# Kernel tuning notes

Measured on AMD Instinct MI355X. Metric: run time of the kernel, lower is better.

Reference implementation:

```python
import jax, jax.numpy as jnp
import numpy as np

N_NODES = 100000


def gcn_conv(h, edge_index, W, b):
    """PyG GCNConv: add self-loops, symmetric normalization, linear transform,
    sum aggregation over incoming edges, plus bias."""
    n = h.shape[0]
    loop = jnp.arange(n)
    row = jnp.concatenate([edge_index[0], loop])  # source nodes
    col = jnp.concatenate([edge_index[1], loop])  # destination nodes
    # degree of destination nodes (edge weight = 1)
    deg = jax.ops.segment_sum(jnp.ones_like(col, dtype=h.dtype), col, num_segments=n)
    dinv = jnp.where(deg > 0, jax.lax.rsqrt(deg), 0.0)
    norm = dinv[row] * dinv[col]  # [E+n]
    hW = h @ W                    # [n, out] small GEMM
    msg = hW[row] * norm[:, None] # gather + scale, [E+n, out]
    out = jax.ops.segment_sum(msg, col, num_segments=n)  # scatter-add
    return out + b


def setup_inputs() -> dict:
    key = jax.random.key(0)
    k1, k2, k3, k4 = jax.random.split(key, 4)
    N, E, D_IN, D_H, D_OUT = N_NODES, 1600000, 64, 64, 32
    x = jax.random.normal(k1, (N, D_IN), dtype=jnp.float32)
    edge_index = jax.random.randint(k2, (2, E), 0, N, dtype=jnp.int64)
    W1 = jax.random.normal(k3, (D_IN, D_H), dtype=jnp.float32) / np.sqrt(D_IN)
    b1 = jnp.zeros((D_H,), dtype=jnp.float32)
    W2 = jax.random.normal(k4, (D_H, D_OUT), dtype=jnp.float32) / np.sqrt(D_H)
    b2 = jnp.zeros((D_OUT,), dtype=jnp.float32)
    return {"x": x, "edge_index": edge_index, "W1": W1, "b1": b1, "W2": W2, "b2": b2}


def reference(x, edge_index, W1, b1, W2, b2):
    # StackedGCNEncoder.encode, eval mode (dropout is identity at inference)
    h = gcn_conv(x, edge_index, W1, b1)
    h = jax.nn.relu(h)
    h = gcn_conv(h, edge_index, W2, b2)
    return h
```

## Files before the change

### kernel.cpp

```cpp
#include <hip/hip_runtime.h>

#define NN 100000
#define NNr 100016
#define NE 1600000
#define STRIDE 48

static __device__ __forceinline__ unsigned short f2bf(float f) {
    unsigned int u = __float_as_uint(f);
    return (unsigned short)((u + 0x7FFFu + ((u >> 16) & 1u)) >> 16);
}
static __device__ __forceinline__ float bflo(unsigned int u) {
    return __uint_as_float(u << 16);
}
static __device__ __forceinline__ float bfhi(unsigned int u) {
    return __uint_as_float(u & 0xFFFF0000u);
}

__global__ void zero_k(int* __restrict__ a, int n) {
    int i = blockIdx.x * blockDim.x + threadIdx.x;
    if (i < n) a[i] = 0;
}

__global__ void dinv_k(const int* __restrict__ cursor, float* __restrict__ dinv, int n) {
    int i = blockIdx.x * blockDim.x + threadIdx.x;
    if (i < n) dinv[i] = rsqrtf((float)cursor[i] + 1.0f);
}

__global__ __launch_bounds__(256) void fused1_k(const float* __restrict__ x,
        const float* __restrict__ W1, unsigned short* __restrict__ A,
        const int* __restrict__ ei, int* __restrict__ cursor,
        int* __restrict__ csr) {
    __shared__ __align__(16) float smem[32 * 68 + 64 * 64];

    if (blockIdx.x & 1) {
        int i = (int)(blockIdx.x >> 1) * 256 + threadIdx.x;
        int2 s = *reinterpret_cast<const int2*>(ei + 2 * i);
        int2 d = *reinterpret_cast<const int2*>(ei + NE + 2 * i);
        int p0 = atomicAdd(&cursor[d.x], 1);
        if (p0 < STRIDE) csr[d.x * STRIDE + p0] = s.x;
        int p1 = atomicAdd(&cursor[d.y], 1);
        if (p1 < STRIDE) csr[d.y * STRIDE + p1] = s.y;
        return;
    }

    float* sH = smem;
    float* sW = smem + 32 * 68;
    const int row0 = (int)(blockIdx.x >> 1) * 32;

    for (int i = threadIdx.x; i < 16 * 64; i += 256)
        *reinterpret_cast<float4*>(&sW[i * 4]) = reinterpret_cast<const float4*>(W1)[i];
    for (int t = threadIdx.x; t < 32 * 16; t += 256) {
        int r = t >> 4, k4 = (t & 15) << 2;
        *reinterpret_cast<float4*>(&sH[r * 68 + k4]) =
            *reinterpret_cast<const float4*>(x + (long long)(row0 + r) * 64 + k4);
    }
    __syncthreads();

    const int tc = threadIdx.x & 15, tr = threadIdx.x >> 4;
    const int rb = tr * 2, cb = tc * 4;
    float acc[2][4] = {};
#pragma unroll
    for (int k = 0; k < 64; k += 4) {
        float a[2][4], w[4][4];
#pragma unroll
        for (int i = 0; i < 2; ++i) {
            float4 t4 = *reinterpret_cast<const float4*>(&sH[(rb + i) * 68 + k]);
            a[i][0] = t4.x; a[i][1] = t4.y; a[i][2] = t4.z; a[i][3] = t4.w;
        }
#pragma unroll
        for (int kk = 0; kk < 4; ++kk) {
            float4 t4 = *reinterpret_cast<const float4*>(&sW[(k + kk) * 64 + cb]);
            w[kk][0] = t4.x; w[kk][1] = t4.y; w[kk][2] = t4.z; w[kk][3] = t4.w;
        }
#pragma unroll
        for (int i = 0; i < 2; ++i)
#pragma unroll
            for (int kk = 0; kk < 4; ++kk)
#pragma unroll
                for (int j = 0; j < 4; ++j)
                    acc[i][j] = fmaf(a[i][kk], w[kk][j], acc[i][j]);
    }
#pragma unroll
    for (int i = 0; i < 2; ++i) {
        ushort4 o;
        o.x = f2bf(acc[i][0]); o.y = f2bf(acc[i][1]);
        o.z = f2bf(acc[i][2]); o.w = f2bf(acc[i][3]);
        *reinterpret_cast<ushort4*>(A + (long long)(row0 + rb + i) * 64 + cb) = o;
    }
}

__global__ __launch_bounds__(256) void gather_gemm2_k(const int* __restrict__ cursor,
        const int* __restrict__ csr, const unsigned int* __restrict__ A32,
        const float* __restrict__ dinv, const float* __restrict__ b1,
        const float* __restrict__ W2, unsigned short* __restrict__ C, int n) {
    __shared__ __align__(16) float sW2[64 * 32];
    __shared__ float sB[4][64];

    for (int i = threadIdx.x; i < 16 * 32; i += 256)
        *reinterpret_cast<float4*>(&sW2[i * 4]) = reinterpret_cast<const float4*>(W2)[i];
    __syncthreads();

    const int wv = threadIdx.x >> 6, lane = threadIdx.x & 63;
    const int half = lane >> 5;
    const int fl = lane & 31;
    const int v = blockIdx.x * 4 + wv;
    if (v >= n) return;

    const int beg = v * STRIDE;
    const int end = beg + min(cursor[v], STRIDE);
    const float dv = dinv[v];
    const unsigned int av = A32[(long long)v * 32 + fl];

    float m0 = 0.0f, m1 = 0.0f;
    int p = beg + half;
    while (p + 6 < end) {
        int r0 = csr[p], r1 = csr[p + 2], r2 = csr[p + 4], r3 = csr[p + 6];
        float n0 = dinv[r0], n1 = dinv[r1], n2 = dinv[r2], n3 = dinv[r3];
        unsigned int a0 = A32[(long long)r0 * 32 + fl];
        unsigned int a1 = A32[(long long)r1 * 32 + fl];
        unsigned int a2 = A32[(long long)r2 * 32 + fl];
        unsigned int a3 = A32[(long long)r3 * 32 + fl];
        m0 = fmaf(bflo(a0), n0, m0); m1 = fmaf(bfhi(a0), n0, m1);
        m0 = fmaf(bflo(a1), n1, m0); m1 = fmaf(bfhi(a1), n1, m1);
        m0 = fmaf(bflo(a2), n2, m0); m1 = fmaf(bfhi(a2), n2, m1);
        m0 = fmaf(bflo(a3), n3, m0); m1 = fmaf(bfhi(a3), n3, m1);
        p += 8;
    }
    while (p < end) {
        int r = csr[p];
        float nr = dinv[r];
        unsigned int a = A32[(long long)r * 32 + fl];
        m0 = fmaf(bflo(a), nr, m0); m1 = fmaf(bfhi(a), nr, m1);
        p += 2;
    }
    m0 += __shfl_xor(m0, 32);
    m1 += __shfl_xor(m1, 32);

    if (half == 0) {
        float2 bb = reinterpret_cast<const float2*>(b1)[fl];
        float B0 = fmaf(dv, fmaf(dv, bflo(av), m0), bb.x);
        float B1 = fmaf(dv, fmaf(dv, bfhi(av), m1), bb.y);
        float2 o; o.x = fmaxf(B0, 0.0f); o.y = fmaxf(B1, 0.0f);
        *reinterpret_cast<float2*>(&sB[wv][2 * fl]) = o;
    }
    __builtin_amdgcn_wave_barrier();

    const int j = lane & 31, kbase = (lane >> 5) << 5;
    float pj = 0.0f;
#pragma unroll
    for (int t = 0; t < 32; ++t) {
        int k = kbase + t;
        pj = fmaf(sB[wv][k], sW2[k * 32 + j], pj);
    }
    pj += __shfl_down(pj, 32);
    if (lane < 32) C[(long long)v * 32 + j] = f2bf(pj);
}

__global__ __launch_bounds__(256) void gather2_k(const int* __restrict__ cursor,
        const int* __restrict__ csr, const unsigned int* __restrict__ C32,
        const float* __restrict__ dinv, const float* __restrict__ b2,
        float* __restrict__ outp, int n) {
    const int wv = threadIdx.x >> 6, lane = threadIdx.x & 63;
    const int q = lane >> 4, fl = lane & 15;
    const int v = blockIdx.x * 4 + wv;
    if (v >= n) return;

    const int beg = v * STRIDE;
    const int end = beg + min(cursor[v], STRIDE);
    const float dv = dinv[v];
    const unsigned int cv = C32[(long long)v * 16 + fl];

    float m0 = 0.0f, m1 = 0.0f;
    int p = beg + q;
    while (p + 12 < end) {
        int r0 = csr[p], r1 = csr[p + 4], r2 = csr[p + 8], r3 = csr[p + 12];
        float n0 = dinv[r0], n1 = dinv[r1], n2 = dinv[r2], n3 = dinv[r3];
        unsigned int c0 = C32[(long long)r0 * 16 + fl];
        unsigned int c1 = C32[(long long)r1 * 16 + fl];
        unsigned int c2 = C32[(long long)r2 * 16 + fl];
        unsigned int c3 = C32[(long long)r3 * 16 + fl];
        m0 = fmaf(bflo(c0), n0, m0); m1 = fmaf(bfhi(c0), n0, m1);
        m0 = fmaf(bflo(c1), n1, m0); m1 = fmaf(bfhi(c1), n1, m1);
        m0 = fmaf(bflo(c2), n2, m0); m1 = fmaf(bfhi(c2), n2, m1);
        m0 = fmaf(bflo(c3), n3, m0); m1 = fmaf(bfhi(c3), n3, m1);
        p += 16;
    }
    while (p < end) {
        int r = csr[p];
        float nr = dinv[r];
        unsigned int c = C32[(long long)r * 16 + fl];
        m0 = fmaf(bflo(c), nr, m0); m1 = fmaf(bfhi(c), nr, m1);
        p += 4;
    }
    m0 += __shfl_xor(m0, 16); m0 += __shfl_xor(m0, 32);
    m1 += __shfl_xor(m1, 16); m1 += __shfl_xor(m1, 32);

    if (q == 0) {
        float2 bb = reinterpret_cast<const float2*>(b2)[fl];
        float2 o;
        o.x = fmaf(dv, fmaf(dv, bflo(cv), m0), bb.x);
        o.y = fmaf(dv, fmaf(dv, bfhi(cv), m1), bb.y);
        reinterpret_cast<float2*>(outp)[(long long)v * 16 + fl] = o;
    }
}

extern "C" void kernel_launch(void* const* d_in, const int* in_sizes, int n_in,
                              void* d_out, int out_size, void* d_ws, size_t ws_size,
                              hipStream_t stream) {
    const float* x  = (const float*)d_in[0];
    const int*   ei = (const int*)d_in[1];
    const float* W1 = (const float*)d_in[2];
    const float* b1 = (const float*)d_in[3];
    const float* W2 = (const float*)d_in[4];
    const float* b2 = (const float*)d_in[5];
    float* out = (float*)d_out;

    int*            cursor = (int*)d_ws;
    int*            csr    = cursor + NNr;
    float*          dinv   = (float*)(csr + NN * STRIDE);
    unsigned short* A      = (unsigned short*)(dinv + NNr);
    unsigned short* C      = A + (long long)NN * 64;

    const int BT = 256;

    zero_k<<<(NN + BT - 1) / BT, BT, 0, stream>>>(cursor, NN);
    fused1_k<<<6250, BT, 0, stream>>>(x, W1, A, ei, cursor, csr);
    dinv_k<<<(NN + BT - 1) / BT, BT, 0, stream>>>(cursor, dinv, NN);
    gather_gemm2_k<<<(NN + 3) / 4, BT, 0, stream>>>(cursor, csr,
        (const unsigned int*)A, dinv, b1, W2, C, NN);
    gather2_k<<<(NN + 3) / 4, BT, 0, stream>>>(cursor, csr,
        (const unsigned int*)C, dinv, b2, out, NN);
}
```

Baseline: 188.8 us.

## Pre-scale features by source dinv and load CSR indices once per wave

Replaces the dinv kernel with a scale pass that multiplies the bf16 hW rows by rsqrt(deg+1) in place. The second layer folds dv into the stored C rows, so neither gather has to fetch dinv[r] for each edge. Each wave also loads its node's CSR row once into lanes and broadcasts indices with shuffles, instead of issuing dependent csr loads per iteration. This drops one random gather per edge, at the cost of an extra read-modify-write over A and a second bf16 rounding of the scaled values.

Result: faster. 174.8 us (-7.4%).

```diff
diff --git a/kernel.cpp b/kernel.cpp
--- a/kernel.cpp
+++ b/kernel.cpp
@@ -15,15 +15,13 @@
 static __device__ __forceinline__ float bfhi(unsigned int u) {
     return __uint_as_float(u & 0xFFFF0000u);
 }
+static __device__ __forceinline__ unsigned int bfpack(float lo, float hi) {
+    return ((unsigned int)f2bf(lo)) | (((unsigned int)f2bf(hi)) << 16);
+}
 
 __global__ void zero_k(int* __restrict__ a, int n) {
     int i = blockIdx.x * blockDim.x + threadIdx.x;
     if (i < n) a[i] = 0;
-}
-
-__global__ void dinv_k(const int* __restrict__ cursor, float* __restrict__ dinv, int n) {
-    int i = blockIdx.x * blockDim.x + threadIdx.x;
-    if (i < n) dinv[i] = rsqrtf((float)cursor[i] + 1.0f);
 }
 
 __global__ __launch_bounds__(256) void fused1_k(const float* __restrict__ x,
@@ -89,10 +87,24 @@
     }
 }
 
+__global__ __launch_bounds__(256) void scale_k(unsigned int* __restrict__ A32,
+        const int* __restrict__ cursor, int n) {
+    int gid = blockIdx.x * blockDim.x + threadIdx.x;
+    if (gid >= n * 8) return;
+    int row = gid >> 3, c = gid & 7;
+    float di = rsqrtf((float)cursor[row] + 1.0f);
+    uint4 u = reinterpret_cast<uint4*>(A32)[(long long)row * 8 + c];
+    u.x = bfpack(bflo(u.x) * di, bfhi(u.x) * di);
+    u.y = bfpack(bflo(u.y) * di, bfhi(u.y) * di);
+    u.z = bfpack(bflo(u.z) * di, bfhi(u.z) * di);
+    u.w = bfpack(bflo(u.w) * di, bfhi(u.w) * di);
+    reinterpret_cast<uint4*>(A32)[(long long)row * 8 + c] = u;
+}
+
 __global__ __launch_bounds__(256) void gather_gemm2_k(const int* __restrict__ cursor,
         const int* __restrict__ csr, const unsigned int* __restrict__ A32,
-        const float* __restrict__ dinv, const float* __restrict__ b1,
-        const float* __restrict__ W2, unsigned short* __restrict__ C, int n) {
+        const float* __restrict__ b1, const float* __restrict__ W2,
+        unsigned short* __restrict__ C, int n) {
     __shared__ __align__(16) float sW2[64 * 32];
     __shared__ float sB[4][64];
 
@@ -106,41 +118,40 @@
     const int v = blockIdx.x * 4 + wv;
     if (v >= n) return;
 
-    const int beg = v * STRIDE;
-    const int end = beg + min(cursor[v], STRIDE);
-    const float dv = dinv[v];
+    const int cv = cursor[v];
+    const int deg = min(cv, STRIDE);
+    const float dv = rsqrtf((float)cv + 1.0f);
+
+    int rl = 0;
+    if (lane < deg) rl = csr[v * STRIDE + lane];
+
     const unsigned int av = A32[(long long)v * 32 + fl];
 
     float m0 = 0.0f, m1 = 0.0f;
-    int p = beg + half;
-    while (p + 6 < end) {
-        int r0 = csr[p], r1 = csr[p + 2], r2 = csr[p + 4], r3 = csr[p + 6];
-        float n0 = dinv[r0], n1 = dinv[r1], n2 = dinv[r2], n3 = dinv[r3];
-        unsigned int a0 = A32[(long long)r0 * 32 + fl];
-        unsigned int a1 = A32[(long long)r1 * 32 + fl];
-        unsigned int a2 = A32[(long long)r2 * 32 + fl];
-        unsigned int a3 = A32[(long long)r3 * 32 + fl];
-        m0 = fmaf(bflo(a0), n0, m0); m1 = fmaf(bfhi(a0), n0, m1);
-        m0 = fmaf(bflo(a1), n1, m0); m1 = fmaf(bfhi(a1), n1, m1);
-        m0 = fmaf(bflo(a2), n2, m0); m1 = fmaf(bfhi(a2), n2, m1);
-        m0 = fmaf(bflo(a3), n3, m0); m1 = fmaf(bfhi(a3), n3, m1);
-        p += 8;
-    }
-    while (p < end) {
-        int r = csr[p];
-        float nr = dinv[r];
-        unsigned int a = A32[(long long)r * 32 + fl];
-        m0 = fmaf(bflo(a), nr, m0); m1 = fmaf(bfhi(a), nr, m1);
-        p += 2;
+    const int T = (deg + 7) >> 3;
+    for (int it = 0; it < T; ++it) {
+        const int e0 = it * 8 + half;
+        int r0 = __shfl(rl, e0);
+        int r1 = __shfl(rl, e0 + 2);
+        int r2 = __shfl(rl, e0 + 4);
+        int r3 = __shfl(rl, e0 + 6);
+        unsigned int a0 = (e0     < deg) ? A32[(long long)r0 * 32 + fl] : 0u;
+        unsigned int a1 = (e0 + 2 < deg) ? A32[(long long)r1 * 32 + fl] : 0u;
+        unsigned int a2 = (e0 + 4 < deg) ? A32[(long long)r2 * 32 + fl] : 0u;
+        unsigned int a3 = (e0 + 6 < deg) ? A32[(long long)r3 * 32 + fl] : 0u;
+        m0 += bflo(a0); m1 += bfhi(a0);
+        m0 += bflo(a1); m1 += bfhi(a1);
+        m0 += bflo(a2); m1 += bfhi(a2);
+        m0 += bflo(a3); m1 += bfhi(a3);
     }
     m0 += __shfl_xor(m0, 32);
     m1 += __shfl_xor(m1, 32);
 
     if (half == 0) {
         float2 bb = reinterpret_cast<const float2*>(b1)[fl];
-        float B0 = fmaf(dv, fmaf(dv, bflo(av), m0), bb.x);
-        float B1 = fmaf(dv, fmaf(dv, bfhi(av), m1), bb.y);
-        float2 o; o.x = fmaxf(B0, 0.0f); o.y = fmaxf(B1, 0.0f);
+        float2 o;
+        o.x = fmaxf(fmaf(dv, m0 + bflo(av), bb.x), 0.0f);
+        o.y = fmaxf(fmaf(dv, m1 + bfhi(av), bb.y), 0.0f);
         *reinterpret_cast<float2*>(&sB[wv][2 * fl]) = o;
     }
     __builtin_amdgcn_wave_barrier();
@@ -153,44 +164,42 @@
         pj = fmaf(sB[wv][k], sW2[k * 32 + j], pj);
     }
     pj += __shfl_down(pj, 32);
-    if (lane < 32) C[(long long)v * 32 + j] = f2bf(pj);
+    if (lane < 32) C[(long long)v * 32 + j] = f2bf(pj * dv);
 }
 
 __global__ __launch_bounds__(256) void gather2_k(const int* __restrict__ cursor,
         const int* __restrict__ csr, const unsigned int* __restrict__ C32,
-        const float* __restrict__ dinv, const float* __restrict__ b2,
-        float* __restrict__ outp, int n) {
+        const float* __restrict__ b2, float* __restrict__ outp, int n) {
     const int wv = threadIdx.x >> 6, lane = threadIdx.x & 63;
     const int q = lane >> 4, fl = lane & 15;
     const int v = blockIdx.x * 4 + wv;
     if (v >= n) return;
 
-    const int beg = v * STRIDE;
-    const int end = beg + min(cursor[v], STRIDE);
-    const float dv = dinv[v];
-    const unsigned int cv = C32[(long long)v * 16 + fl];
-
+    const int cv = cursor[v];
+    const int deg = min(cv, STRIDE);
+    const float dv = rsqrtf((float)cv + 1.0f);
+
+    int rl = 0;
+    if (lane < deg) rl = csr[v * STRIDE + lane];
+
+    const unsigned int cvu = C32[(long long)v * 16 + fl];
     float m0 = 0.0f, m1 = 0.0f;
-    int p = beg + q;
-    while (p + 12 < end) {
-        int r0 = csr[p], r1 = csr[p + 4], r2 = csr[p + 8], r3 = csr[p + 12];
-        float n0 = dinv[r0], n1 = dinv[r1], n2 = dinv[r2], n3 = dinv[r3];
-        unsigned int c0 = C32[(long long)r0 * 16 + fl];
-        unsigned int c1 = C32[(long long)r1 * 16 + fl];
-        unsigned int c2 = C32[(long long)r2 * 16 + fl];
-        unsigned int c3 = C32[(long long)r3 * 16 + fl];
-        m0 = fmaf(bflo(c0), n0, m0); m1 = fmaf(bfhi(c0), n0, m1);
-        m0 = fmaf(bflo(c1), n1, m0); m1 = fmaf(bfhi(c1), n1, m1);
-        m0 = fmaf(bflo(c2), n2, m0); m1 = fmaf(bfhi(c2), n2, m1);
-        m0 = fmaf(bflo(c3), n3, m0); m1 = fmaf(bfhi(c3), n3, m1);
-        p += 16;
-    }
-    while (p < end) {
-        int r = csr[p];
-        float nr = dinv[r];
-        unsigned int c = C32[(long long)r * 16 + fl];
-        m0 = fmaf(bflo(c), nr, m0); m1 = fmaf(bfhi(c), nr, m1);
-        p += 4;
+
+    const int T = (deg + 15) >> 4;
+    for (int it = 0; it < T; ++it) {
+        const int e0 = it * 16 + q;
+        int r0 = __shfl(rl, e0);
+        int r1 = __shfl(rl, e0 + 4);
+        int r2 = __shfl(rl, e0 + 8);
+        int r3 = __shfl(rl, e0 + 12);
+        unsigned int c0 = (e0      < deg) ? C32[(long long)r0 * 16 + fl] : 0u;
+        unsigned int c1 = (e0 + 4  < deg) ? C32[(long long)r1 * 16 + fl] : 0u;
+        unsigned int c2 = (e0 + 8  < deg) ? C32[(long long)r2 * 16 + fl] : 0u;
+        unsigned int c3 = (e0 + 12 < deg) ? C32[(long long)r3 * 16 + fl] : 0u;
+        m0 += bflo(c0); m1 += bfhi(c0);
+        m0 += bflo(c1); m1 += bfhi(c1);
+        m0 += bflo(c2); m1 += bfhi(c2);
+        m0 += bflo(c3); m1 += bfhi(c3);
     }
     m0 += __shfl_xor(m0, 16); m0 += __shfl_xor(m0, 32);
     m1 += __shfl_xor(m1, 16); m1 += __shfl_xor(m1, 32);
@@ -198,8 +207,8 @@
     if (q == 0) {
         float2 bb = reinterpret_cast<const float2*>(b2)[fl];
         float2 o;
-        o.x = fmaf(dv, fmaf(dv, bflo(cv), m0), bb.x);
-        o.y = fmaf(dv, fmaf(dv, bfhi(cv), m1), bb.y);
+        o.x = fmaf(dv, m0 + bflo(cvu), bb.x);
+        o.y = fmaf(dv, m1 + bfhi(cvu), bb.y);
         reinterpret_cast<float2*>(outp)[(long long)v * 16 + fl] = o;
     }
 }
@@ -217,17 +226,16 @@
 
     int*            cursor = (int*)d_ws;
     int*            csr    = cursor + NNr;
-    float*          dinv   = (float*)(csr + NN * STRIDE);
-    unsigned short* A      = (unsigned short*)(dinv + NNr);
+    unsigned short* A      = (unsigned short*)(csr + NN * STRIDE);
     unsigned short* C      = A + (long long)NN * 64;
 
     const int BT = 256;
 
     zero_k<<<(NN + BT - 1) / BT, BT, 0, stream>>>(cursor, NN);
     fused1_k<<<6250, BT, 0, stream>>>(x, W1, A, ei, cursor, csr);
-    dinv_k<<<(NN + BT - 1) / BT, BT, 0, stream>>>(cursor, dinv, NN);
+    scale_k<<<(NN * 8 + BT - 1) / BT, BT, 0, stream>>>((unsigned int*)A, cursor, NN);
     gather_gemm2_k<<<(NN + 3) / 4, BT, 0, stream>>>(cursor, csr,
-        (const unsigned int*)A, dinv, b1, W2, C, NN);
+        (const unsigned int*)A, b1, W2, C, NN);
     gather2_k<<<(NN + 3) / 4, BT, 0, stream>>>(cursor, csr,
-        (const unsigned int*)C, dinv, b2, out, NN);
-}
+        (const unsigned int*)C, b2, out, NN);
+}
```
